# Kernel optimization log

Measured on AMD Instinct MI355X. Metric: run time of the kernel, lower is better.

Reference implementation:

```python
import jax, jax.numpy as jnp
import numpy as np

B, N, F, U = 4, 4096, 128, 64
BN_EPS = 1e-3  # Keras BatchNormalization default epsilon
NEG_BIG = -9e15


def setup_inputs() -> dict:
    key = jax.random.key(0)
    k1, k2, k3, k4 = jax.random.split(key, 4)
    return {
        "h": jax.random.normal(k1, (B, N, F), dtype=jnp.float32),
        "adj": jax.random.randint(k2, (B, N, N), 0, 2, dtype=jnp.int32),
        "W": jax.random.normal(k3, (F, U), dtype=jnp.float32) * (1.0 / np.sqrt(F)),
        "a": jax.random.normal(k4, (2 * U, 1), dtype=jnp.float32) * (1.0 / np.sqrt(2 * U)),
        "gamma": jnp.ones((U,), dtype=jnp.float32),
        "beta": jnp.zeros((U,), dtype=jnp.float32),
        "moving_mean": jnp.zeros((U,), dtype=jnp.float32),
        "moving_var": jnp.ones((U,), dtype=jnp.float32),
    }


def reference(h, adj, W, a, gamma, beta, moving_mean, moving_var):
    # Wh: [B, N, U]
    Wh = jnp.einsum("bnf,fu->bnu", h, W)
    U_ = W.shape[1]
    a1, a2 = a[:U_, 0], a[U_:, 0]  # each [U]
    # e[b,i,j] = leaky_relu(Wh[b,i]@a1 + Wh[b,j]@a2) -- avoids O(N^2*2U) concat
    src = jnp.einsum("bnu,u->bn", Wh, a1)  # [B, N]
    dst = jnp.einsum("bnu,u->bn", Wh, a2)  # [B, N]
    e = src[:, :, None] + dst[:, None, :]  # [B, N, N]
    e = jnp.where(e >= 0, e, 0.2 * e)  # LeakyReLU(alpha=0.2)
    e = jnp.where(adj > 0, e, jnp.asarray(NEG_BIG, e.dtype))
    attention = jax.nn.softmax(e, axis=-1)  # [B, N, N]
    out = jnp.einsum("bij,bju->biu", attention, Wh)  # [B, N, U]
    # BatchNorm in inference mode (training flag not passed in call())
    inv = jax.lax.rsqrt(moving_var + BN_EPS)
    out = (out - moving_mean) * inv * gamma + beta
    return jax.nn.relu(out)
```

## Files before the change

kernel.cpp:

```cpp
#include <hip/hip_runtime.h>
#include <hip/hip_bf16.h>

#define BB 4
#define NN 4096
#define FF 128
#define UU 64
#define LOG2E 1.4426950408889634f

typedef float  f32x4   __attribute__((ext_vector_type(4)));
typedef __bf16 bf16x8  __attribute__((ext_vector_type(8)));
typedef int    int4v   __attribute__((ext_vector_type(4)));
typedef float  flt4v   __attribute__((ext_vector_type(4)));
typedef unsigned short us4 __attribute__((ext_vector_type(4)));

__device__ __forceinline__ unsigned short f2bf(float x) {
    unsigned u = __float_as_uint(x);
    u += 0x7FFFu + ((u >> 16) & 1u);
    return (unsigned short)(u >> 16);
}

__device__ __forceinline__ float fexp2(float x) {
#if defined(__has_builtin)
# if __has_builtin(__builtin_amdgcn_exp2f)
    return __builtin_amdgcn_exp2f(x);
# else
    return exp2f(x);
# endif
#else
    return exp2f(x);
#endif
}

__global__ __launch_bounds__(256) void prep_kernel(
    const float* __restrict__ h, const float* __restrict__ W,
    const float* __restrict__ a,
    unsigned short* __restrict__ WhT, float* __restrict__ src, float* __restrict__ dst)
{
    __shared__ float Wl[FF][UU];
    __shared__ unsigned short tile[16][UU];
    const int t = threadIdx.x, w = t >> 6, l = t & 63;
    const int bid = blockIdx.x;
    const int b = bid >> 8;
    const int i0 = (bid & 255) << 4;

    {
        const flt4v* Wv = (const flt4v*)W;
        flt4v* Wlv = (flt4v*)&Wl[0][0];
        #pragma unroll
        for (int k = 0; k < 8; ++k) Wlv[t + 256 * k] = Wv[t + 256 * k];
    }
    __syncthreads();

    float acc[4] = {0.f, 0.f, 0.f, 0.f};
    const float* hrow = h + ((size_t)(b * NN + i0 + w * 4) * FF);
    #pragma unroll 8
    for (int fc = 0; fc < 32; ++fc) {
        const int f0 = fc << 2;
        flt4v h0 = *(const flt4v*)(hrow + f0);
        flt4v h1 = *(const flt4v*)(hrow + FF + f0);
        flt4v h2 = *(const flt4v*)(hrow + 2 * FF + f0);
        flt4v h3 = *(const flt4v*)(hrow + 3 * FF + f0);
        #pragma unroll
        for (int e = 0; e < 4; ++e) {
            float wv = Wl[f0 + e][l];
            acc[0] += h0[e] * wv;
            acc[1] += h1[e] * wv;
            acc[2] += h2[e] * wv;
            acc[3] += h3[e] * wv;
        }
    }

    float a1 = a[l], a2 = a[UU + l];
    #pragma unroll
    for (int k = 0; k < 4; ++k) {
        float s = acc[k] * a1, d = acc[k] * a2;
        #pragma unroll
        for (int off = 32; off > 0; off >>= 1) {
            s += __shfl_xor(s, off, 64);
            d += __shfl_xor(d, off, 64);
        }
        int i = i0 + w * 4 + k;
        if (l == 0) {
            src[b * NN + i] = s * LOG2E;
            dst[b * NN + i] = d * LOG2E;
        }
        tile[w * 4 + k][l] = f2bf(acc[k]);
    }
    __syncthreads();

    {
        int u = t >> 2, ic = (t & 3) << 2;
        us4 vv = { tile[ic + 0][u], tile[ic + 1][u], tile[ic + 2][u], tile[ic + 3][u] };
        *(us4*)(WhT + ((size_t)(b * UU + u) * NN) + i0 + ic) = vv;
    }
}

#define MFMA16(A, B, C) __builtin_amdgcn_mfma_f32_16x16x32_bf16(A, B, C, 0, 0, 0)

__global__ __launch_bounds__(256, 4) void gat_kernel(
    const int* __restrict__ adj, const unsigned short* __restrict__ WhT,
    const float* __restrict__ src, const float* __restrict__ dst,
    const float* __restrict__ gamma, const float* __restrict__ beta,
    const float* __restrict__ mmean, const float* __restrict__ mvar,
    float* __restrict__ out)
{
    __shared__ float opart[4][16][UU];
    __shared__ float lpart[4][16];
    const int t = threadIdx.x, w = t >> 6, l = t & 63;
    const int bid = blockIdx.x;
    const int b = bid >> 8;
    const int i0 = (bid & 255) << 4;
    const int row = l & 15;
    const int kg = l >> 4;
    const int ko = kg << 3;
    const int i = i0 + row;

    const float srow = src[b * NN + i];
    const int* adjr = adj + ((size_t)(b * NN + i) << 12);
    const float* dstb = dst + b * NN;
    const unsigned short* w0 = WhT + ((size_t)(b * UU + row) * NN);

    f32x4 acc0 = {0,0,0,0}, acc1 = {0,0,0,0}, acc2 = {0,0,0,0}, acc3 = {0,0,0,0};
    float ls0 = 0.f, ls1 = 0.f;

    int4v Pa, Pb, Pc, Pd, Qa, Qb, Qc, Qd;

    #define LDADJ(va, vb, vc, vd, bs)                       \
    {                                                       \
        va = *(const int4v*)(adjr + (bs) + ko);             \
        vb = *(const int4v*)(adjr + (bs) + ko + 4);         \
        vc = *(const int4v*)(adjr + (bs) + ko + 32);        \
        vd = *(const int4v*)(adjr + (bs) + ko + 36);        \
    }
    #define PACK(va, vb, vc, vd, m0, m1)                                 \
    {                                                                    \
        m0 = (unsigned)(va[0] | (va[1] << 1) | (va[2] << 2) | (va[3] << 3) \
           | (vb[0] << 4) | (vb[1] << 5) | (vb[2] << 6) | (vb[3] << 7)); \
        m1 = (unsigned)(vc[0] | (vc[1] << 1) | (vc[2] << 2) | (vc[3] << 3) \
           | (vd[0] << 4) | (vd[1] << 5) | (vd[2] << 6) | (vd[3] << 7)); \
    }

    #define PE(af, e, Dv, ei, m, ls)                                \
    {                                                               \
        float tt = srow + Dv[ei];                                   \
        tt = fmaxf(tt, 0.2f * tt);      \
        float pp = fexp2(tt);                                       \
        pp = (m & (1u << e)) ? pp : 0.0f;                           \
        ls += pp;                                                   \
        af[e] = (__bf16)pp;                                         \
    }

    auto body = [&](int bs, unsigned m0, unsigned m1) {
        const flt4v  D0a = *(const flt4v*)(dstb + bs + ko);
        const flt4v  D0b = *(const flt4v*)(dstb + bs + ko + 4);
        const bf16x8 B00 = *(const bf16x8*)(w0 + bs + ko);
        const bf16x8 B01 = *(const bf16x8*)(w0 + 16 * NN + bs + ko);
        const bf16x8 B02 = *(const bf16x8*)(w0 + 32 * NN + bs + ko);
        const bf16x8 B03 = *(const bf16x8*)(w0 + 48 * NN + bs + ko);
        bf16x8 af0;
        PE(af0, 0, D0a, 0, m0, ls0) PE(af0, 1, D0a, 1, m0, ls0)
        PE(af0, 2, D0a, 2, m0, ls0) PE(af0, 3, D0a, 3, m0, ls0)
        PE(af0, 4, D0b, 0, m0, ls0) PE(af0, 5, D0b, 1, m0, ls0)
        PE(af0, 6, D0b, 2, m0, ls0) PE(af0, 7, D0b, 3, m0, ls0)
        acc0 = MFMA16(af0, B00, acc0);
        acc1 = MFMA16(af0, B01, acc1);
        acc2 = MFMA16(af0, B02, acc2);
        acc3 = MFMA16(af0, B03, acc3);
        const flt4v  D1a = *(const flt4v*)(dstb + bs + ko + 32);
        const flt4v  D1b = *(const flt4v*)(dstb + bs + ko + 36);
        const bf16x8 B10 = *(const bf16x8*)(w0 + bs + ko + 32);
        const bf16x8 B11 = *(const bf16x8*)(w0 + 16 * NN + bs + ko + 32);
        const bf16x8 B12 = *(const bf16x8*)(w0 + 32 * NN + bs + ko + 32);
        const bf16x8 B13 = *(const bf16x8*)(w0 + 48 * NN + bs + ko + 32);
        bf16x8 af1;
        PE(af1, 0, D1a, 0, m1, ls1) PE(af1, 1, D1a, 1, m1, ls1)
        PE(af1, 2, D1a, 2, m1, ls1) PE(af1, 3, D1a, 3, m1, ls1)
        PE(af1, 4, D1b, 0, m1, ls1) PE(af1, 5, D1b, 1, m1, ls1)
        PE(af1, 6, D1b, 2, m1, ls1) PE(af1, 7, D1b, 3, m1, ls1)
        acc0 = MFMA16(af1, B10, acc0);
        acc1 = MFMA16(af1, B11, acc1);
        acc2 = MFMA16(af1, B12, acc2);
        acc3 = MFMA16(af1, B13, acc3);
    };

    int bs = w << 6;
    LDADJ(Pa, Pb, Pc, Pd, bs)
    LDADJ(Qa, Qb, Qc, Qd, bs + 256)

    for (int it = 0; it < 16; it += 2) {
        unsigned m0, m1;
        PACK(Pa, Pb, Pc, Pd, m0, m1)
        if (it < 14) LDADJ(Pa, Pb, Pc, Pd, bs + 512)
        body(bs, m0, m1);
        PACK(Qa, Qb, Qc, Qd, m0, m1)
        if (it < 13) LDADJ(Qa, Qb, Qc, Qd, bs + 768)
        body(bs + 256, m0, m1);
        bs += 512;
    }
    #undef PE
    #undef LDADJ
    #undef PACK

    float lsum = ls0 + ls1;
    lsum += __shfl_xor(lsum, 16, 64);
    lsum += __shfl_xor(lsum, 32, 64);
    if (l < 16) lpart[w][l] = lsum;

    #pragma unroll
    for (int r = 0; r < 4; ++r) {
        opart[w][kg * 4 + r][      row] = acc0[r];
        opart[w][kg * 4 + r][16 + row] = acc1[r];
        opart[w][kg * 4 + r][32 + row] = acc2[r];
        opart[w][kg * 4 + r][48 + row] = acc3[r];
    }
    __syncthreads();

    const int u = t & 63;
    const float inv = rsqrtf(mvar[u] + 1e-3f);
    const float sc = gamma[u] * inv;
    const float bi = beta[u] - mmean[u] * sc;
    const int ib = (t >> 6) << 2;
    #pragma unroll
    for (int r = 0; r < 4; ++r) {
        int il = ib + r;
        float ltot = lpart[0][il] + lpart[1][il] + lpart[2][il] + lpart[3][il];
        float v = opart[0][il][u] + opart[1][il][u] + opart[2][il][u] + opart[3][il][u];
        v = v / ltot * sc + bi;
        out[((size_t)(b * NN + i0 + il) << 6) + u] = fmaxf(v, 0.f);
    }
}

extern "C" void kernel_launch(void* const* d_in, const int* in_sizes, int n_in,
                              void* d_out, int out_size, void* d_ws, size_t ws_size,
                              hipStream_t stream) {
    const float* h     = (const float*)d_in[0];
    const int*   adj   = (const int*)  d_in[1];
    const float* W     = (const float*)d_in[2];
    const float* a     = (const float*)d_in[3];
    const float* gamma = (const float*)d_in[4];
    const float* beta  = (const float*)d_in[5];
    const float* mmean = (const float*)d_in[6];
    const float* mvar  = (const float*)d_in[7];
    float* out = (float*)d_out;

    unsigned short* WhT = (unsigned short*)d_ws;
    float* src = (float*)((char*)d_ws + (size_t)2 * 1024 * 1024);
    float* dst = src + BB * NN;

    prep_kernel<<<BB * (NN / 16), 256, 0, stream>>>(h, W, a, WhT, src, dst);
    gat_kernel<<<BB * (NN / 16), 256, 0, stream>>>(adj, WhT, src, dst,
                                                   gamma, beta, mmean, mvar, out);
}
```

Baseline: 426.8 us.

## Pre-pack adjacency into bitmasks in a separate kernel before attention

Adds a pack_kernel that reads the int32 adjacency once, coalesced, and uses wavefront ballots to build a 64-bit mask per 64 columns. The attention kernel then loads compact 32-bit mask words instead of streaming int32 adjacency inside its MFMA loop, and the manual adjacency prefetch pipeline is dropped. The full 256 MB adjacency read still happens, now in a separate launch, and the packed mask is written and read back. The main loop loses its software prefetch of the mask data.

New measurement: 467.9 us. 1.1x slower.

```diff
diff --git a/kernel.cpp b/kernel.cpp
--- a/kernel.cpp
+++ b/kernel.cpp
@@ -9,7 +9,6 @@
 
 typedef float  f32x4   __attribute__((ext_vector_type(4)));
 typedef __bf16 bf16x8  __attribute__((ext_vector_type(8)));
-typedef int    int4v   __attribute__((ext_vector_type(4)));
 typedef float  flt4v   __attribute__((ext_vector_type(4)));
 typedef unsigned short us4 __attribute__((ext_vector_type(4)));
 
@@ -29,6 +28,22 @@
 #else
     return exp2f(x);
 #endif
+}
+
+__global__ __launch_bounds__(256) void pack_kernel(
+    const int* __restrict__ adj, unsigned long long* __restrict__ mask64)
+{
+    const int t = threadIdx.x, l = t & 63;
+    const int row = blockIdx.x * 4 + (t >> 6);
+    const int* rp = adj + ((size_t)row << 12);
+    unsigned long long mine = 0;
+    #pragma unroll 8
+    for (int c = 0; c < 64; ++c) {
+        int v = rp[c * 64 + l];
+        unsigned long long bal = __ballot(v != 0);
+        if (l == c) mine = bal;
+    }
+    mask64[((size_t)row << 6) + l] = mine;
 }
 
 __global__ __launch_bounds__(256) void prep_kernel(
@@ -98,7 +113,7 @@
 #define MFMA16(A, B, C) __builtin_amdgcn_mfma_f32_16x16x32_bf16(A, B, C, 0, 0, 0)
 
 __global__ __launch_bounds__(256, 4) void gat_kernel(
-    const int* __restrict__ adj, const unsigned short* __restrict__ WhT,
+    const unsigned* __restrict__ mask, const unsigned short* __restrict__ WhT,
     const float* __restrict__ src, const float* __restrict__ dst,
     const float* __restrict__ gamma, const float* __restrict__ beta,
     const float* __restrict__ mmean, const float* __restrict__ mvar,
@@ -113,32 +128,16 @@
     const int row = l & 15;
     const int kg = l >> 4;
     const int ko = kg << 3;
+    const int ksh = kg << 3;
     const int i = i0 + row;
 
     const float srow = src[b * NN + i];
-    const int* adjr = adj + ((size_t)(b * NN + i) << 12);
+    const unsigned* mrow = mask + ((size_t)(b * NN + i) << 7);
     const float* dstb = dst + b * NN;
     const unsigned short* w0 = WhT + ((size_t)(b * UU + row) * NN);
 
     f32x4 acc0 = {0,0,0,0}, acc1 = {0,0,0,0}, acc2 = {0,0,0,0}, acc3 = {0,0,0,0};
     float ls0 = 0.f, ls1 = 0.f;
-
-    int4v Pa, Pb, Pc, Pd, Qa, Qb, Qc, Qd;
-
-    #define LDADJ(va, vb, vc, vd, bs)                       \
-    {                                                       \
-        va = *(const int4v*)(adjr + (bs) + ko);             \
-        vb = *(const int4v*)(adjr + (bs) + ko + 4);         \
-        vc = *(const int4v*)(adjr + (bs) + ko + 32);        \
-        vd = *(const int4v*)(adjr + (bs) + ko + 36);        \
-    }
-    #define PACK(va, vb, vc, vd, m0, m1)                                 \
-    {                                                                    \
-        m0 = (unsigned)(va[0] | (va[1] << 1) | (va[2] << 2) | (va[3] << 3) \
-           | (vb[0] << 4) | (vb[1] << 5) | (vb[2] << 6) | (vb[3] << 7)); \
-        m1 = (unsigned)(vc[0] | (vc[1] << 1) | (vc[2] << 2) | (vc[3] << 3) \
-           | (vd[0] << 4) | (vd[1] << 5) | (vd[2] << 6) | (vd[3] << 7)); \
-    }
 
     #define PE(af, e, Dv, ei, m, ls)                                \
     {                                                               \
@@ -150,7 +149,10 @@
         af[e] = (__bf16)pp;                                         \
     }
 
-    auto body = [&](int bs, unsigned m0, unsigned m1) {
+    for (int it = 0; it < 16; ++it) {
+        const int bs = (w << 6) + (it << 8);
+        const unsigned m0 = (mrow[(bs >> 5)    ] >> ksh) & 0xffu;
+        const unsigned m1 = (mrow[(bs >> 5) + 1] >> ksh) & 0xffu;
         const flt4v  D0a = *(const flt4v*)(dstb + bs + ko);
         const flt4v  D0b = *(const flt4v*)(dstb + bs + ko + 4);
         const bf16x8 B00 = *(const bf16x8*)(w0 + bs + ko);
@@ -181,25 +183,8 @@
         acc1 = MFMA16(af1, B11, acc1);
         acc2 = MFMA16(af1, B12, acc2);
         acc3 = MFMA16(af1, B13, acc3);
-    };
-
-    int bs = w << 6;
-    LDADJ(Pa, Pb, Pc, Pd, bs)
-    LDADJ(Qa, Qb, Qc, Qd, bs + 256)
-
-    for (int it = 0; it < 16; it += 2) {
-        unsigned m0, m1;
-        PACK(Pa, Pb, Pc, Pd, m0, m1)
-        if (it < 14) LDADJ(Pa, Pb, Pc, Pd, bs + 512)
-        body(bs, m0, m1);
-        PACK(Qa, Qb, Qc, Qd, m0, m1)
-        if (it < 13) LDADJ(Qa, Qb, Qc, Qd, bs + 768)
-        body(bs + 256, m0, m1);
-        bs += 512;
     }
     #undef PE
-    #undef LDADJ
-    #undef PACK
 
     float lsum = ls0 + ls1;
     lsum += __shfl_xor(lsum, 16, 64);
@@ -246,8 +231,12 @@
     unsigned short* WhT = (unsigned short*)d_ws;
     float* src = (float*)((char*)d_ws + (size_t)2 * 1024 * 1024);
     float* dst = src + BB * NN;
-
+    unsigned long long* mask64 =
+        (unsigned long long*)((char*)d_ws + (size_t)4 * 1024 * 1024);
+
+    pack_kernel<<<BB * NN / 4, 256, 0, stream>>>(adj, mask64);
     prep_kernel<<<BB * (NN / 16), 256, 0, stream>>>(h, W, a, WhT, src, dst);
-    gat_kernel<<<BB * (NN / 16), 256, 0, stream>>>(adj, WhT, src, dst,
-                                                   gamma, beta, mmean, mvar, out);
-}
+    gat_kernel<<<BB * (NN / 16), 256, 0, stream>>>((const unsigned*)mask64, WhT,
+                                                   src, dst, gamma, beta,
+                                                   mmean, mvar, out);
+}
```
